# Kernel tuning notes

Hardware: AMD Instinct MI355X
Metric: run time of the kernel (lower is better)

Reference implementation:

```python
import jax, jax.numpy as jnp
import numpy as np
import math

INPUTDIM = 256
OUTDIM = 512
GRIDSIZE = 64

def setup_inputs() -> dict:
    key = jax.random.key(0)
    k1, k2 = jax.random.split(key)
    x = jax.random.normal(k1, (4096, INPUTDIM), dtype=jnp.float32)
    # init: randn / (sqrt(inputdim) * sqrt(gridsize))  (smooth_initialization=False)
    fouriercoeffs = jax.random.normal(k2, (2, OUTDIM, INPUTDIM, GRIDSIZE), dtype=jnp.float32) / (
        math.sqrt(INPUTDIM) * math.sqrt(GRIDSIZE))
    bias = jnp.zeros((1, OUTDIM), dtype=jnp.float32)
    return {"x": x, "fouriercoeffs": fouriercoeffs, "bias": bias}

def reference(x, fouriercoeffs, bias):
    # x: [N, I]; fouriercoeffs: [2, O, I, G]; bias: [1, O]
    k = jnp.arange(1, GRIDSIZE + 1, dtype=x.dtype)          # [G]
    kx = x[:, :, None] * k[None, None, :]                   # [N, I, G]
    c = jnp.cos(kx)
    s = jnp.sin(kx)
    # contraction over (I, G) — GEMM-equivalent of the naive broadcast-sum
    y = jnp.einsum('nig,oig->no', c, fouriercoeffs[0])
    y = y + jnp.einsum('nig,oig->no', s, fouriercoeffs[1])
    y = y + bias
    return y
```

## Files before the change

### kernel.cpp

```cpp
#include <hip/hip_runtime.h>
#include <hip/hip_bf16.h>

#define IDIM 256
#define GDIM 64
#define ODIM 512
#define KD   (IDIM * GDIM)
#define TILE_SHORTS (512 * 64)
#define WS_NEED ((size_t)512 * TILE_SHORTS * 2)

typedef __attribute__((ext_vector_type(8))) short bhalf8;
typedef __attribute__((ext_vector_type(4))) float fvec4;
typedef __attribute__((ext_vector_type(4))) unsigned uvec4;

#define INV2PI 0.15915494309189535f

static __device__ __forceinline__ short bf16b(float v) {
    __hip_bfloat16 hb = __float2bfloat16(v);
    short s; __builtin_memcpy(&s, &hb, 2); return s;
}
static __device__ __forceinline__ unsigned cvtpk(float lo, float hi) {
    unsigned r;
    asm("v_cvt_pk_bf16_f32 %0, %1, %2" : "=v"(r) : "v"(lo), "v"(hi));
    return r;
}

__global__ void prep_b(const float* __restrict__ coeffs, short* __restrict__ ws) {
    const int b = blockIdx.x;
    const int i = b >> 1, h = b & 1;
    const int o = threadIdx.x;
    short* dst = ws + ((size_t)b * 512 + o) * 64;
    const int swz = (o & 7) << 4;
#pragma unroll
    for (int j = 0; j < 8; ++j) {
        const int z = j >> 2, Qq = j & 3;
        const float* src = coeffs + ((size_t)z * ODIM + o) * KD
                         + (size_t)i * GDIM + 16 * Qq + 8 * h;
        fvec4 v0 = ((const fvec4*)src)[0];
        fvec4 v1 = ((const fvec4*)src)[1];
        bhalf8 pk;
#pragma unroll
        for (int u = 0; u < 4; ++u) { pk[u] = bf16b(v0[u]); pk[4 + u] = bf16b(v1[u]); }
        *(bhalf8*)((char*)dst + ((j * 16) ^ swz)) = pk;
    }
}

__global__ void bias_init(const float* __restrict__ bias, float* __restrict__ out) {
    int idx = blockIdx.x * 256 + threadIdx.x;
    fvec4 bv = ((const fvec4*)bias)[idx & 127];
    ((fvec4*)out)[idx] = bv;
}

#define FENCE() do { asm volatile("s_waitcnt vmcnt(0) lgkmcnt(0)" ::: "memory"); \
                     __builtin_amdgcn_sched_barrier(0); \
                     __syncthreads(); } while (0)

#define ADV2(cA,cB,sA,sB,C2) do { \
    float _cn = __builtin_fmaf((C2),(cB),-(cA)); (cA)=(cB); (cB)=_cn; \
    float _sn = __builtin_fmaf((C2),(sB),-(sA)); (sA)=(sB); (sB)=_sn; \
    _cn = __builtin_fmaf((C2),(cB),-(cA)); (cA)=(cB); (cB)=_cn; \
    _sn = __builtin_fmaf((C2),(sB),-(sA)); (sA)=(sB); (sB)=_sn; } while (0)

template<int USE_WS>
__global__ void __launch_bounds__(256, 4)
fkan_gemm(const float* __restrict__ x, const float* __restrict__ coeffs,
          const short* __restrict__ wsb, float* __restrict__ out) {
    __shared__ __align__(16) short B_lds[2][128 * 64];
    __shared__ float  sl_rev[4][128];
    __shared__ float2 sl_cs[4][128];

    const int bx = blockIdx.x;
    const int xcd = bx & 7, j = bx >> 3;
    const int lg  = xcd * 4 + (j & 3);
    const int mt  = j >> 2;
    const int ot  = lg >> 3, ks = lg & 7;
    const int row0 = mt * 128, col0 = ot * 128;
    const int i0 = ks * 32;

    const int t = threadIdx.x;
    const int lane = t & 63, wid = t >> 6;
    const int kl  = (lane >> 4) * 16;
    const int msk = (lane & 7) << 4;
    const int rA0 = wid * 32 + (lane & 15);
    const float m0f = (float)(16 * (lane >> 4) + 1);

    fvec4 acc[2][8];
#pragma unroll
    for (int a = 0; a < 2; ++a)
#pragma unroll
        for (int b = 0; b < 8; ++b) acc[a][b] = (fvec4)0.0f;

    auto fill_sl = [&](int chunk) {
#pragma unroll
        for (int w = 0; w < 2; ++w) {
            int idx = t + w * 256;
            int il2 = idx & 3, r2 = idx >> 2;
            float xv = x[(size_t)(row0 + r2) * IDIM + i0 + chunk * 4 + il2];
            float rev = xv * INV2PI;
            float a = __builtin_amdgcn_fractf(rev);
            float2 cs;
            cs.x = __builtin_amdgcn_cosf(a);
            cs.y = __builtin_amdgcn_sinf(a);
            sl_rev[il2][r2] = rev;
            sl_cs[il2][r2] = cs;
        }
    };

    auto dmaB = [&](int T1) {
        const short* src = wsb + (size_t)(i0 * 2 + T1) * TILE_SHORTS
                         + (size_t)col0 * 64 + (size_t)t * 8;
        const int bsel = T1 & 1;
#pragma unroll
        for (int q = 0; q < 4; ++q)
            __builtin_amdgcn_global_load_lds(
                (const __attribute__((address_space(1))) unsigned*)(src + q * 2048),
                (__attribute__((address_space(3))) unsigned*)
                    &B_lds[bsel][q * 2048 + wid * 512],
                16, 0, 0);
    };

    auto stage_fb = [&](int T1) {
        const int bsel = T1 & 1;
        const int i = i0 + (T1 >> 1), hh = T1 & 1;
        const int o = t >> 1, z = t & 1;
        char* drow = (char*)&B_lds[bsel][o * 64];
        const int swz = (o & 7) << 4;
#pragma unroll
        for (int Qq = 0; Qq < 4; ++Qq) {
            const float* src = coeffs + ((size_t)z * ODIM + col0 + o) * KD
                             + (size_t)i * GDIM + 16 * Qq + 8 * hh;
            fvec4 v0 = ((const fvec4*)src)[0];
            fvec4 v1 = ((const fvec4*)src)[1];
            bhalf8 pk;
#pragma unroll
            for (int u = 0; u < 4; ++u) { pk[u] = bf16b(v0[u]); pk[4 + u] = bf16b(v1[u]); }
            *(bhalf8*)(drow + ((z * 64 + Qq * 16) ^ swz)) = pk;
        }
    };

    fill_sl(0);
    if (USE_WS) dmaB(0);
    FENCE();

    float ccA0, ccB0, csA0, csB0, cC20;
    float ccA1, ccB1, csA1, csB1, cC21;

#pragma unroll 1
    for (int T = 0; T < 64; ++T) {
        if ((T & 7) == 0 && T > 0) {
            fill_sl(T >> 3);
            FENCE();
        }
        if (USE_WS) {
            if (T < 63) dmaB(T + 1);
            __builtin_amdgcn_sched_barrier(0);
        } else {
            stage_fb(T);
            FENCE();
        }

        const int bsel = T & 1;
        const int il = (T >> 1) & 3;
        const short* Bb = &B_lds[bsel][0];

        bhalf8 afc[2], afs[2];
        if ((T & 1) == 0) {
#pragma unroll
            for (int fm = 0; fm < 2; ++fm) {
                const int rr = rA0 + fm * 16;
                float rev = sl_rev[il][rr];
                float2 cs1 = sl_cs[il][rr];
                float C2 = cs1.x + cs1.x;
                float a0 = __builtin_amdgcn_fractf(rev * m0f);
                float cA = __builtin_amdgcn_cosf(a0);
                float sA = __builtin_amdgcn_sinf(a0);
                float cB = __builtin_fmaf(cA, cs1.x, -(sA * cs1.y));
                float sB = __builtin_fmaf(sA, cs1.x,  (cA * cs1.y));
                uvec4 uc, us;
                uc[0] = cvtpk(cA, cB); us[0] = cvtpk(sA, sB);
#pragma unroll
                for (int p = 1; p < 4; ++p) {
                    ADV2(cA, cB, sA, sB, C2);
                    uc[p] = cvtpk(cA, cB); us[p] = cvtpk(sA, sB);
                }
                if (fm == 0) { ccA0 = cA; ccB0 = cB; csA0 = sA; csB0 = sB; cC20 = C2; }
                else         { ccA1 = cA; ccB1 = cB; csA1 = sA; csB1 = sB; cC21 = C2; }
                afc[fm] = __builtin_bit_cast(bhalf8, uc);
                afs[fm] = __builtin_bit_cast(bhalf8, us);
            }
        } else {
#pragma unroll
            for (int fm = 0; fm < 2; ++fm) {
                float cA = fm ? ccA1 : ccA0, cB = fm ? ccB1 : ccB0;
                float sA = fm ? csA1 : csA0, sB = fm ? csB1 : csB0;
                float C2 = fm ? cC21 : cC20;
                uvec4 uc, us;
#pragma unroll
                for (int p = 0; p < 4; ++p) {
                    ADV2(cA, cB, sA, sB, C2);
                    uc[p] = cvtpk(cA, cB); us[p] = cvtpk(sA, sB);
                }
                afc[fm] = __builtin_bit_cast(bhalf8, uc);
                afs[fm] = __builtin_bit_cast(bhalf8, us);
            }
        }

#pragma unroll
        for (int half = 0; half < 2; ++half) {
            bhalf8 bq[4];
#pragma unroll
            for (int f4 = 0; f4 < 4; ++f4)
                bq[f4] = *(const bhalf8*)((const char*)Bb +
                    (size_t)(half * 64 + f4 * 16 + (lane & 15)) * 128 + (kl ^ msk));
            __builtin_amdgcn_s_setprio(1);
#pragma unroll
            for (int fm = 0; fm < 2; ++fm)
#pragma unroll
                for (int f4 = 0; f4 < 4; ++f4)
                    acc[fm][half * 4 + f4] = __builtin_amdgcn_mfma_f32_16x16x32_bf16(
                        afc[fm], bq[f4], acc[fm][half * 4 + f4], 0, 0, 0);
            __builtin_amdgcn_s_setprio(0);
#pragma unroll
            for (int f4 = 0; f4 < 4; ++f4)
                bq[f4] = *(const bhalf8*)((const char*)Bb +
                    (size_t)(half * 64 + f4 * 16 + (lane & 15)) * 128 + ((64 + kl) ^ msk));
            __builtin_amdgcn_s_setprio(1);
#pragma unroll
            for (int fm = 0; fm < 2; ++fm)
#pragma unroll
                for (int f4 = 0; f4 < 4; ++f4)
                    acc[fm][half * 4 + f4] = __builtin_amdgcn_mfma_f32_16x16x32_bf16(
                        afs[fm], bq[f4], acc[fm][half * 4 + f4], 0, 0, 0);
            __builtin_amdgcn_s_setprio(0);
        }

        FENCE();
    }

#pragma unroll
    for (int fm = 0; fm < 2; ++fm) {
#pragma unroll
        for (int f = 0; f < 8; ++f) {
            int col = col0 + f * 16 + (lane & 15);
#pragma unroll
            for (int r = 0; r < 4; ++r) {
                int row = row0 + wid * 32 + fm * 16 + ((lane >> 4) * 4) + r;
                atomicAdd(&out[(size_t)row * ODIM + col], acc[fm][f][r]);
            }
        }
    }
}

extern "C" void kernel_launch(void* const* d_in, const int* in_sizes, int n_in,
                              void* d_out, int out_size, void* d_ws, size_t ws_size,
                              hipStream_t stream) {
    (void)in_sizes; (void)n_in; (void)out_size;
    const float* x      = (const float*)d_in[0];
    const float* coeffs = (const float*)d_in[1];
    const float* bias   = (const float*)d_in[2];
    float* out = (float*)d_out;

    const bool use_ws = (ws_size >= WS_NEED) && (((uintptr_t)d_ws & 15) == 0);

    bias_init<<<dim3(2048), dim3(256), 0, stream>>>(bias, out);
    if (use_ws) {
        prep_b<<<dim3(512), dim3(512), 0, stream>>>(coeffs, (short*)d_ws);
        fkan_gemm<1><<<dim3(1024), dim3(256), 0, stream>>>(x, coeffs, (const short*)d_ws, out);
    } else {
        fkan_gemm<0><<<dim3(1024), dim3(256), 0, stream>>>(x, coeffs, nullptr, out);
    }
}
```

Baseline: 176.7 us.

## Split B tiles into cos/sin halves with 4-deep LDS ring and vmcnt-based pipelining

Restructures the GEMM main loop to stream B in cos and sin half-tiles through a 4-slot LDS ring. Each slot is issued two steps ahead and waited on with partial vmcnt waits plus a bare s_barrier, instead of a full vmcnt/lgkmcnt drain each iteration. The workspace layout and swizzle are changed to 64-byte rows with a 2-bit XOR key, and the cos and sin recurrences are interleaved per half. The aim is to overlap global-to-LDS DMA with MFMA work and cut full-drain barriers. The cost is more barriers per iteration and subtler ordering between the ring slots.

```diff
diff --git a/kernel.cpp b/kernel.cpp
--- a/kernel.cpp
+++ b/kernel.cpp
@@ -5,14 +5,15 @@
 #define GDIM 64
 #define ODIM 512
 #define KD   (IDIM * GDIM)
-#define TILE_SHORTS (512 * 64)
-#define WS_NEED ((size_t)512 * TILE_SHORTS * 2)
+#define WS_NEED ((size_t)512 * 512 * 64 * 2)
 
 typedef __attribute__((ext_vector_type(8))) short bhalf8;
 typedef __attribute__((ext_vector_type(4))) float fvec4;
 typedef __attribute__((ext_vector_type(4))) unsigned uvec4;
 
 #define INV2PI 0.15915494309189535f
+#define AS1 __attribute__((address_space(1)))
+#define AS3 __attribute__((address_space(3)))
 
 static __device__ __forceinline__ short bf16b(float v) {
     __hip_bfloat16 hb = __float2bfloat16(v);
@@ -24,24 +25,37 @@
     return r;
 }
 
+#define ADVP(A,B,C2) do { float _t = __builtin_fmaf((C2),(B),-(A)); (A)=(B); (B)=_t; \
+                          _t = __builtin_fmaf((C2),(B),-(A)); (A)=(B); (B)=_t; } while (0)
+
+#define BOUND(N) do { asm volatile("s_waitcnt vmcnt(" #N ")" ::: "memory"); \
+                      __builtin_amdgcn_sched_barrier(0); \
+                      __builtin_amdgcn_s_barrier(); \
+                      __builtin_amdgcn_sched_barrier(0); } while (0)
+#define BOUND_LG() do { asm volatile("s_waitcnt lgkmcnt(0)" ::: "memory"); \
+                      __builtin_amdgcn_sched_barrier(0); \
+                      __builtin_amdgcn_s_barrier(); \
+                      __builtin_amdgcn_sched_barrier(0); } while (0)
+
 __global__ void prep_b(const float* __restrict__ coeffs, short* __restrict__ ws) {
     const int b = blockIdx.x;
     const int i = b >> 1, h = b & 1;
     const int o = threadIdx.x;
-    short* dst = ws + ((size_t)b * 512 + o) * 64;
-    const int swz = (o & 7) << 4;
-#pragma unroll
-    for (int j = 0; j < 8; ++j) {
-        const int z = j >> 2, Qq = j & 3;
-        const float* src = coeffs + ((size_t)z * ODIM + o) * KD
-                         + (size_t)i * GDIM + 16 * Qq + 8 * h;
-        fvec4 v0 = ((const fvec4*)src)[0];
-        fvec4 v1 = ((const fvec4*)src)[1];
-        bhalf8 pk;
-#pragma unroll
-        for (int u = 0; u < 4; ++u) { pk[u] = bf16b(v0[u]); pk[4 + u] = bf16b(v1[u]); }
-        *(bhalf8*)((char*)dst + ((j * 16) ^ swz)) = pk;
-    }
+    char* dst = (char*)(ws + ((size_t)b * 512 + o) * 64);
+    const int key = (o >> 1) & 3;
+#pragma unroll
+    for (int z = 0; z < 2; ++z)
+#pragma unroll
+        for (int g = 0; g < 4; ++g) {
+            const float* src = coeffs + ((size_t)z * ODIM + o) * KD
+                             + (size_t)i * GDIM + 16 * g + 8 * h;
+            fvec4 v0 = ((const fvec4*)src)[0];
+            fvec4 v1 = ((const fvec4*)src)[1];
+            bhalf8 pk;
+#pragma unroll
+            for (int u = 0; u < 4; ++u) { pk[u] = bf16b(v0[u]); pk[4 + u] = bf16b(v1[u]); }
+            *(bhalf8*)(dst + z * 64 + (((g ^ key)) << 4)) = pk;
+        }
 }
 
 __global__ void bias_init(const float* __restrict__ bias, float* __restrict__ out) {
@@ -50,21 +64,11 @@
     ((fvec4*)out)[idx] = bv;
 }
 
-#define FENCE() do { asm volatile("s_waitcnt vmcnt(0) lgkmcnt(0)" ::: "memory"); \
-                     __builtin_amdgcn_sched_barrier(0); \
-                     __syncthreads(); } while (0)
-
-#define ADV2(cA,cB,sA,sB,C2) do { \
-    float _cn = __builtin_fmaf((C2),(cB),-(cA)); (cA)=(cB); (cB)=_cn; \
-    float _sn = __builtin_fmaf((C2),(sB),-(sA)); (sA)=(sB); (sB)=_sn; \
-    _cn = __builtin_fmaf((C2),(cB),-(cA)); (cA)=(cB); (cB)=_cn; \
-    _sn = __builtin_fmaf((C2),(sB),-(sA)); (sA)=(sB); (sB)=_sn; } while (0)
-
 template<int USE_WS>
 __global__ void __launch_bounds__(256, 4)
 fkan_gemm(const float* __restrict__ x, const float* __restrict__ coeffs,
           const short* __restrict__ wsb, float* __restrict__ out) {
-    __shared__ __align__(16) short B_lds[2][128 * 64];
+    __shared__ __align__(16) short B4[4][4096];
     __shared__ float  sl_rev[4][128];
     __shared__ float2 sl_cs[4][128];
 
@@ -78,10 +82,10 @@
 
     const int t = threadIdx.x;
     const int lane = t & 63, wid = t >> 6;
-    const int kl  = (lane >> 4) * 16;
-    const int msk = (lane & 7) << 4;
+    const int q   = lane >> 4;
+    const int key = ((lane & 15) >> 1) & 3;
     const int rA0 = wid * 32 + (lane & 15);
-    const float m0f = (float)(16 * (lane >> 4) + 1);
+    const float m0f = (float)(16 * q + 1);
 
     fvec4 acc[2][8];
 #pragma unroll
@@ -105,135 +109,168 @@
         }
     };
 
-    auto dmaB = [&](int T1) {
-        const short* src = wsb + (size_t)(i0 * 2 + T1) * TILE_SHORTS
-                         + (size_t)col0 * 64 + (size_t)t * 8;
-        const int bsel = T1 & 1;
-#pragma unroll
-        for (int q = 0; q < 4; ++q)
-            __builtin_amdgcn_global_load_lds(
-                (const __attribute__((address_space(1))) unsigned*)(src + q * 2048),
-                (__attribute__((address_space(3))) unsigned*)
-                    &B_lds[bsel][q * 2048 + wid * 512],
-                16, 0, 0);
+    auto dma_half = [&](int Hh) {
+        const int Tt = Hh >> 1, zz = Hh & 1, bs = Hh & 3;
+        const char* srcl = (const char*)wsb + (((size_t)(i0 * 2 + Tt)) << 16)
+                         + (size_t)(col0 + wid * 32 + (lane >> 2)) * 128
+                         + zz * 64 + (lane & 3) * 16;
+        __builtin_amdgcn_global_load_lds((const AS1 unsigned*)srcl,
+            (AS3 unsigned*)&B4[bs][wid * 1024], 16, 0, 0);
+        __builtin_amdgcn_global_load_lds((const AS1 unsigned*)(srcl + 16 * 128),
+            (AS3 unsigned*)&B4[bs][wid * 1024 + 512], 16, 0, 0);
     };
 
-    auto stage_fb = [&](int T1) {
-        const int bsel = T1 & 1;
-        const int i = i0 + (T1 >> 1), hh = T1 & 1;
-        const int o = t >> 1, z = t & 1;
-        char* drow = (char*)&B_lds[bsel][o * 64];
-        const int swz = (o & 7) << 4;
-#pragma unroll
-        for (int Qq = 0; Qq < 4; ++Qq) {
-            const float* src = coeffs + ((size_t)z * ODIM + col0 + o) * KD
-                             + (size_t)i * GDIM + 16 * Qq + 8 * hh;
+    auto stage_fb = [&](int Tt) {
+        const int hh = Tt & 1, i = i0 + (Tt >> 1);
+        const int o = t >> 1, zz = t & 1;
+        const int keyo = (o >> 1) & 3;
+        char* d0 = (char*)&B4[(2 * Tt + zz) & 3][o * 32];
+#pragma unroll
+        for (int g = 0; g < 4; ++g) {
+            const float* src = coeffs + ((size_t)zz * ODIM + col0 + o) * KD
+                             + (size_t)i * GDIM + 16 * g + 8 * hh;
             fvec4 v0 = ((const fvec4*)src)[0];
             fvec4 v1 = ((const fvec4*)src)[1];
             bhalf8 pk;
 #pragma unroll
             for (int u = 0; u < 4; ++u) { pk[u] = bf16b(v0[u]); pk[4 + u] = bf16b(v1[u]); }
-            *(bhalf8*)(drow + ((z * 64 + Qq * 16) ^ swz)) = pk;
+            *(bhalf8*)(d0 + ((g ^ keyo) << 4)) = pk;
         }
     };
 
+    auto mfma_half = [&](int bs, bhalf8 af0, bhalf8 af1) {
+        const char* Bb = (const char*)&B4[bs][0];
+        const int goff = (q ^ key) << 4;
+#pragma unroll
+        for (int ch = 0; ch < 2; ++ch) {
+            bhalf8 bq[4];
+#pragma unroll
+            for (int j2 = 0; j2 < 4; ++j2)
+                bq[j2] = *(const bhalf8*)(Bb +
+                    (size_t)((lane & 15) + (ch * 4 + j2) * 16) * 64 + goff);
+            __builtin_amdgcn_s_setprio(1);
+#pragma unroll
+            for (int j2 = 0; j2 < 4; ++j2) {
+                acc[0][ch * 4 + j2] = __builtin_amdgcn_mfma_f32_16x16x32_bf16(
+                    af0, bq[j2], acc[0][ch * 4 + j2], 0, 0, 0);
+                acc[1][ch * 4 + j2] = __builtin_amdgcn_mfma_f32_16x16x32_bf16(
+                    af1, bq[j2], acc[1][ch * 4 + j2], 0, 0, 0);
+            }
+            __builtin_amdgcn_s_setprio(0);
+        }
+    };
+
+    float ccA0, ccB0, ccA1, ccB1;
+    float ssA0, ssB0, ssA1, ssB1;
+    float C20, C21;
+
     fill_sl(0);
-    if (USE_WS) dmaB(0);
-    FENCE();
-
-    float ccA0, ccB0, csA0, csB0, cC20;
-    float ccA1, ccB1, csA1, csB1, cC21;
+    if (USE_WS) {
+        dma_half(0); dma_half(1);
+        BOUND(2);
+    } else {
+        stage_fb(0);
+        __syncthreads();
+    }
 
 #pragma unroll 1
-    for (int T = 0; T < 64; ++T) {
-        if ((T & 7) == 0 && T > 0) {
-            fill_sl(T >> 3);
-            FENCE();
-        }
+    for (int H4 = 0; H4 < 32; ++H4) {
+        const int Hb = H4 * 4;
+        const int il = H4 & 3;
+        bhalf8 af[2];
+
         if (USE_WS) {
-            if (T < 63) dmaB(T + 1);
-            __builtin_amdgcn_sched_barrier(0);
+            if (Hb > 0) {
+                if ((Hb & 15) == 0) {
+                    BOUND(2);
+                    fill_sl(Hb >> 4);
+                    BOUND_LG();
+                } else {
+                    BOUND(2);
+                }
+            }
+            dma_half(Hb + 2);
         } else {
-            stage_fb(T);
-            FENCE();
-        }
-
-        const int bsel = T & 1;
-        const int il = (T >> 1) & 3;
-        const short* Bb = &B_lds[bsel][0];
-
-        bhalf8 afc[2], afs[2];
-        if ((T & 1) == 0) {
-#pragma unroll
-            for (int fm = 0; fm < 2; ++fm) {
-                const int rr = rA0 + fm * 16;
-                float rev = sl_rev[il][rr];
-                float2 cs1 = sl_cs[il][rr];
-                float C2 = cs1.x + cs1.x;
-                float a0 = __builtin_amdgcn_fractf(rev * m0f);
-                float cA = __builtin_amdgcn_cosf(a0);
-                float sA = __builtin_amdgcn_sinf(a0);
-                float cB = __builtin_fmaf(cA, cs1.x, -(sA * cs1.y));
-                float sB = __builtin_fmaf(sA, cs1.x,  (cA * cs1.y));
-                uvec4 uc, us;
-                uc[0] = cvtpk(cA, cB); us[0] = cvtpk(sA, sB);
-#pragma unroll
-                for (int p = 1; p < 4; ++p) {
-                    ADV2(cA, cB, sA, sB, C2);
-                    uc[p] = cvtpk(cA, cB); us[p] = cvtpk(sA, sB);
-                }
-                if (fm == 0) { ccA0 = cA; ccB0 = cB; csA0 = sA; csB0 = sB; cC20 = C2; }
-                else         { ccA1 = cA; ccB1 = cB; csA1 = sA; csB1 = sB; cC21 = C2; }
-                afc[fm] = __builtin_bit_cast(bhalf8, uc);
-                afs[fm] = __builtin_bit_cast(bhalf8, us);
+            if (Hb > 0) {
+                __syncthreads();
+                if ((Hb & 15) == 0) fill_sl(Hb >> 4);
+                stage_fb(Hb >> 1);
+                __syncthreads();
             }
+        }
+#pragma unroll
+        for (int fm = 0; fm < 2; ++fm) {
+            const int rr = rA0 + fm * 16;
+            float rev = sl_rev[il][rr];
+            float2 cs1 = sl_cs[il][rr];
+            float C2x = cs1.x + cs1.x;
+            float a0 = __builtin_amdgcn_fractf(rev * m0f);
+            float c0 = __builtin_amdgcn_cosf(a0);
+            float s0 = __builtin_amdgcn_sinf(a0);
+            float cBv = __builtin_fmaf(c0, cs1.x, -(s0 * cs1.y));
+            float sBv = __builtin_fmaf(s0, cs1.x,  c0 * cs1.y);
+            uvec4 u; u[0] = cvtpk(c0, cBv);
+            float A = c0, B = cBv;
+            ADVP(A, B, C2x); u[1] = cvtpk(A, B);
+            ADVP(A, B, C2x); u[2] = cvtpk(A, B);
+            ADVP(A, B, C2x); u[3] = cvtpk(A, B);
+            if (fm == 0) { ccA0 = A; ccB0 = B; ssA0 = s0; ssB0 = sBv; C20 = C2x; }
+            else         { ccA1 = A; ccB1 = B; ssA1 = s0; ssB1 = sBv; C21 = C2x; }
+            af[fm] = __builtin_bit_cast(bhalf8, u);
+        }
+        mfma_half(Hb & 3, af[0], af[1]);
+
+        if (USE_WS) { BOUND(2); dma_half(Hb + 3); }
+#pragma unroll
+        for (int fm = 0; fm < 2; ++fm) {
+            float A = fm ? ssA1 : ssA0, B = fm ? ssB1 : ssB0;
+            float C2x = fm ? C21 : C20;
+            uvec4 u; u[0] = cvtpk(A, B);
+            ADVP(A, B, C2x); u[1] = cvtpk(A, B);
+            ADVP(A, B, C2x); u[2] = cvtpk(A, B);
+            ADVP(A, B, C2x); u[3] = cvtpk(A, B);
+            if (fm == 0) { ssA0 = A; ssB0 = B; } else { ssA1 = A; ssB1 = B; }
+            af[fm] = __builtin_bit_cast(bhalf8, u);
+        }
+        mfma_half((Hb + 1) & 3, af[0], af[1]);
+
+        if (USE_WS) {
+            BOUND(2);
+            if (Hb + 4 < 128) dma_half(Hb + 4);
         } else {
-#pragma unroll
-            for (int fm = 0; fm < 2; ++fm) {
-                float cA = fm ? ccA1 : ccA0, cB = fm ? ccB1 : ccB0;
-                float sA = fm ? csA1 : csA0, sB = fm ? csB1 : csB0;
-                float C2 = fm ? cC21 : cC20;
-                uvec4 uc, us;
-#pragma unroll
-                for (int p = 0; p < 4; ++p) {
-                    ADV2(cA, cB, sA, sB, C2);
-                    uc[p] = cvtpk(cA, cB); us[p] = cvtpk(sA, sB);
-                }
-                afc[fm] = __builtin_bit_cast(bhalf8, uc);
-                afs[fm] = __builtin_bit_cast(bhalf8, us);
-            }
-        }
-
-#pragma unroll
-        for (int half = 0; half < 2; ++half) {
-            bhalf8 bq[4];
-#pragma unroll
-            for (int f4 = 0; f4 < 4; ++f4)
-                bq[f4] = *(const bhalf8*)((const char*)Bb +
-                    (size_t)(half * 64 + f4 * 16 + (lane & 15)) * 128 + (kl ^ msk));
-            __builtin_amdgcn_s_setprio(1);
-#pragma unroll
-            for (int fm = 0; fm < 2; ++fm)
-#pragma unroll
-                for (int f4 = 0; f4 < 4; ++f4)
-                    acc[fm][half * 4 + f4] = __builtin_amdgcn_mfma_f32_16x16x32_bf16(
-                        afc[fm], bq[f4], acc[fm][half * 4 + f4], 0, 0, 0);
-            __builtin_amdgcn_s_setprio(0);
-#pragma unroll
-            for (int f4 = 0; f4 < 4; ++f4)
-                bq[f4] = *(const bhalf8*)((const char*)Bb +
-                    (size_t)(half * 64 + f4 * 16 + (lane & 15)) * 128 + ((64 + kl) ^ msk));
-            __builtin_amdgcn_s_setprio(1);
-#pragma unroll
-            for (int fm = 0; fm < 2; ++fm)
-#pragma unroll
-                for (int f4 = 0; f4 < 4; ++f4)
-                    acc[fm][half * 4 + f4] = __builtin_amdgcn_mfma_f32_16x16x32_bf16(
-                        afs[fm], bq[f4], acc[fm][half * 4 + f4], 0, 0, 0);
-            __builtin_amdgcn_s_setprio(0);
-        }
-
-        FENCE();
+            __syncthreads();
+            stage_fb((Hb >> 1) + 1);
+            __syncthreads();
+        }
+#pragma unroll
+        for (int fm = 0; fm < 2; ++fm) {
+            float A = fm ? ccA1 : ccA0, B = fm ? ccB1 : ccB0;
+            float C2x = fm ? C21 : C20;
+            uvec4 u;
+            ADVP(A, B, C2x); u[0] = cvtpk(A, B);
+            ADVP(A, B, C2x); u[1] = cvtpk(A, B);
+            ADVP(A, B, C2x); u[2] = cvtpk(A, B);
+            ADVP(A, B, C2x); u[3] = cvtpk(A, B);
+            af[fm] = __builtin_bit_cast(bhalf8, u);
+        }
+        mfma_half((Hb + 2) & 3, af[0], af[1]);
+
+        if (USE_WS) {
+            BOUND(2);
+            if (Hb + 5 < 128) dma_half(Hb + 5);
+        }
+#pragma unroll
+        for (int fm = 0; fm < 2; ++fm) {
+            float A = fm ? ssA1 : ssA0, B = fm ? ssB1 : ssB0;
+            float C2x = fm ? C21 : C20;
+            uvec4 u;
+            ADVP(A, B, C2x); u[0] = cvtpk(A, B);
+            ADVP(A, B, C2x); u[1] = cvtpk(A, B);
+            ADVP(A, B, C2x); u[2] = cvtpk(A, B);
+            ADVP(A, B, C2x); u[3] = cvtpk(A, B);
+            af[fm] = __builtin_bit_cast(bhalf8, u);
+        }
+        mfma_half((Hb + 3) & 3, af[0], af[1]);
     }
 
 #pragma unroll
```

Result: slower. 190.1 us (+7.6%).

## Software-pipeline cos/sin generation with MFMA and make sine table per-wave

Applied to the files above, without the earlier changes.

Restructures the main loop so the cosine A-fragments for the next step are generated after the current step's MFMAs, and the sine fragments are computed between the cosine and sine MFMA batches. This interleaves VALU recurrence work with matrix work. The per-chunk fill of the sine/cosine seed table now covers only each wave's own rows and is issued two steps ahead, which removes its extra block barrier. Register pressure rises because the fragments and recurrence state stay live across iterations, and the recurrence order changes slightly.

```diff
diff --git a/kernel.cpp b/kernel.cpp
--- a/kernel.cpp
+++ b/kernel.cpp
@@ -13,6 +13,8 @@
 typedef __attribute__((ext_vector_type(4))) unsigned uvec4;
 
 #define INV2PI 0.15915494309189535f
+#define AS1 __attribute__((address_space(1)))
+#define AS3 __attribute__((address_space(3)))
 
 static __device__ __forceinline__ short bf16b(float v) {
     __hip_bfloat16 hb = __float2bfloat16(v);
@@ -23,6 +25,9 @@
     asm("v_cvt_pk_bf16_f32 %0, %1, %2" : "=v"(r) : "v"(lo), "v"(hi));
     return r;
 }
+
+#define ADVP(A,B,C2) do { float _t = __builtin_fmaf((C2),(B),-(A)); (A)=(B); (B)=_t; \
+                          _t = __builtin_fmaf((C2),(B),-(A)); (A)=(B); (B)=_t; } while (0)
 
 __global__ void prep_b(const float* __restrict__ coeffs, short* __restrict__ ws) {
     const int b = blockIdx.x;
@@ -54,12 +59,6 @@
                      __builtin_amdgcn_sched_barrier(0); \
                      __syncthreads(); } while (0)
 
-#define ADV2(cA,cB,sA,sB,C2) do { \
-    float _cn = __builtin_fmaf((C2),(cB),-(cA)); (cA)=(cB); (cB)=_cn; \
-    float _sn = __builtin_fmaf((C2),(sB),-(sA)); (sA)=(sB); (sB)=_sn; \
-    _cn = __builtin_fmaf((C2),(cB),-(cA)); (cA)=(cB); (cB)=_cn; \
-    _sn = __builtin_fmaf((C2),(sB),-(sA)); (sA)=(sB); (sB)=_sn; } while (0)
-
 template<int USE_WS>
 __global__ void __launch_bounds__(256, 4)
 fkan_gemm(const float* __restrict__ x, const float* __restrict__ coeffs,
@@ -91,9 +90,9 @@
 
     auto fill_sl = [&](int chunk) {
 #pragma unroll
-        for (int w = 0; w < 2; ++w) {
-            int idx = t + w * 256;
-            int il2 = idx & 3, r2 = idx >> 2;
+        for (int w2 = 0; w2 < 2; ++w2) {
+            int idx = lane + w2 * 64;
+            int il2 = idx & 3, r2 = wid * 32 + (idx >> 2);
             float xv = x[(size_t)(row0 + r2) * IDIM + i0 + chunk * 4 + il2];
             float rev = xv * INV2PI;
             float a = __builtin_amdgcn_fractf(rev);
@@ -112,9 +111,8 @@
 #pragma unroll
         for (int q = 0; q < 4; ++q)
             __builtin_amdgcn_global_load_lds(
-                (const __attribute__((address_space(1))) unsigned*)(src + q * 2048),
-                (__attribute__((address_space(3))) unsigned*)
-                    &B_lds[bsel][q * 2048 + wid * 512],
+                (const AS1 unsigned*)(src + q * 2048),
+                (AS3 unsigned*)&B_lds[bsel][q * 2048 + wid * 512],
                 16, 0, 0);
     };
 
@@ -137,103 +135,124 @@
         }
     };
 
+    float ccA0, ccB0, ccA1, ccB1;
+    float ssA0, ssB0, ssA1, ssB1;
+    float C20, C21;
+    bhalf8 afc[2], afs[2];
+
+    auto seed_even = [&](int Te) {
+        const int il = (Te >> 1) & 3;
+#pragma unroll
+        for (int fm = 0; fm < 2; ++fm) {
+            const int rr = rA0 + fm * 16;
+            float rev = sl_rev[il][rr];
+            float2 cs1 = sl_cs[il][rr];
+            float C2x = cs1.x + cs1.x;
+            float a0 = __builtin_amdgcn_fractf(rev * m0f);
+            float c0 = __builtin_amdgcn_cosf(a0);
+            float s0 = __builtin_amdgcn_sinf(a0);
+            float cBv = __builtin_fmaf(c0, cs1.x, -(s0 * cs1.y));
+            float sBv = __builtin_fmaf(s0, cs1.x,  c0 * cs1.y);
+            uvec4 u; u[0] = cvtpk(c0, cBv);
+            float A = c0, B = cBv;
+            ADVP(A, B, C2x); u[1] = cvtpk(A, B);
+            ADVP(A, B, C2x); u[2] = cvtpk(A, B);
+            ADVP(A, B, C2x); u[3] = cvtpk(A, B);
+            if (fm == 0) { ccA0 = A; ccB0 = B; ssA0 = s0; ssB0 = sBv; C20 = C2x; }
+            else         { ccA1 = A; ccB1 = B; ssA1 = s0; ssB1 = sBv; C21 = C2x; }
+            afc[fm] = __builtin_bit_cast(bhalf8, u);
+        }
+    };
+
+    auto mfma_z = [&](const char* Bb, int z, bhalf8 a0f, bhalf8 a1f) {
+        const int koff = (z * 64 + kl) ^ msk;
+#pragma unroll
+        for (int half = 0; half < 2; ++half) {
+            bhalf8 bq[4];
+#pragma unroll
+            for (int f4 = 0; f4 < 4; ++f4)
+                bq[f4] = *(const bhalf8*)(Bb +
+                    (size_t)(half * 64 + f4 * 16 + (lane & 15)) * 128 + koff);
+            __builtin_amdgcn_s_setprio(1);
+#pragma unroll
+            for (int f4 = 0; f4 < 4; ++f4) {
+                acc[0][half * 4 + f4] = __builtin_amdgcn_mfma_f32_16x16x32_bf16(
+                    a0f, bq[f4], acc[0][half * 4 + f4], 0, 0, 0);
+                acc[1][half * 4 + f4] = __builtin_amdgcn_mfma_f32_16x16x32_bf16(
+                    a1f, bq[f4], acc[1][half * 4 + f4], 0, 0, 0);
+            }
+            __builtin_amdgcn_s_setprio(0);
+        }
+    };
+
     fill_sl(0);
-    if (USE_WS) dmaB(0);
-    FENCE();
-
-    float ccA0, ccB0, csA0, csB0, cC20;
-    float ccA1, ccB1, csA1, csB1, cC21;
+    asm volatile("s_waitcnt lgkmcnt(0)" ::: "memory");
+    __builtin_amdgcn_sched_barrier(0);
+    seed_even(0);
+    if (USE_WS) { dmaB(0); FENCE(); }
+    else        { __syncthreads(); }
 
 #pragma unroll 1
     for (int T = 0; T < 64; ++T) {
-        if ((T & 7) == 0 && T > 0) {
-            fill_sl(T >> 3);
-            FENCE();
-        }
         if (USE_WS) {
+            if ((T & 7) == 6 && T < 62) fill_sl((T + 2) >> 3);
             if (T < 63) dmaB(T + 1);
             __builtin_amdgcn_sched_barrier(0);
         } else {
+            if ((T & 7) == 6 && T < 62) fill_sl((T + 2) >> 3);
             stage_fb(T);
-            FENCE();
-        }
-
-        const int bsel = T & 1;
-        const int il = (T >> 1) & 3;
-        const short* Bb = &B_lds[bsel][0];
-
-        bhalf8 afc[2], afs[2];
+            __syncthreads();
+        }
+
+        const char* Bb = (const char*)&B_lds[T & 1][0];
+
+        mfma_z(Bb, 0, afc[0], afc[1]);
         if ((T & 1) == 0) {
 #pragma unroll
             for (int fm = 0; fm < 2; ++fm) {
-                const int rr = rA0 + fm * 16;
-                float rev = sl_rev[il][rr];
-                float2 cs1 = sl_cs[il][rr];
-                float C2 = cs1.x + cs1.x;
-                float a0 = __builtin_amdgcn_fractf(rev * m0f);
-                float cA = __builtin_amdgcn_cosf(a0);
-                float sA = __builtin_amdgcn_sinf(a0);
-                float cB = __builtin_fmaf(cA, cs1.x, -(sA * cs1.y));
-                float sB = __builtin_fmaf(sA, cs1.x,  (cA * cs1.y));
-                uvec4 uc, us;
-                uc[0] = cvtpk(cA, cB); us[0] = cvtpk(sA, sB);
-#pragma unroll
-                for (int p = 1; p < 4; ++p) {
-                    ADV2(cA, cB, sA, sB, C2);
-                    uc[p] = cvtpk(cA, cB); us[p] = cvtpk(sA, sB);
+                float A = fm ? ssA1 : ssA0, B = fm ? ssB1 : ssB0;
+                float C2x = fm ? C21 : C20;
+                uvec4 u; u[0] = cvtpk(A, B);
+                ADVP(A, B, C2x); u[1] = cvtpk(A, B);
+                ADVP(A, B, C2x); u[2] = cvtpk(A, B);
+                ADVP(A, B, C2x); u[3] = cvtpk(A, B);
+                if (fm == 0) { ssA0 = A; ssB0 = B; } else { ssA1 = A; ssB1 = B; }
+                afs[fm] = __builtin_bit_cast(bhalf8, u);
+            }
+        } else {
+#pragma unroll
+            for (int fm = 0; fm < 2; ++fm) {
+                float A = fm ? ssA1 : ssA0, B = fm ? ssB1 : ssB0;
+                float C2x = fm ? C21 : C20;
+                uvec4 u;
+                ADVP(A, B, C2x); u[0] = cvtpk(A, B);
+                ADVP(A, B, C2x); u[1] = cvtpk(A, B);
+                ADVP(A, B, C2x); u[2] = cvtpk(A, B);
+                ADVP(A, B, C2x); u[3] = cvtpk(A, B);
+                afs[fm] = __builtin_bit_cast(bhalf8, u);
+            }
+        }
+
+        mfma_z(Bb, 1, afs[0], afs[1]);
+        if (T < 63) {
+            if ((T & 1) == 0) {
+#pragma unroll
+                for (int fm = 0; fm < 2; ++fm) {
+                    float A = fm ? ccA1 : ccA0, B = fm ? ccB1 : ccB0;
+                    float C2x = fm ? C21 : C20;
+                    uvec4 u;
+                    ADVP(A, B, C2x); u[0] = cvtpk(A, B);
+                    ADVP(A, B, C2x); u[1] = cvtpk(A, B);
+                    ADVP(A, B, C2x); u[2] = cvtpk(A, B);
+                    ADVP(A, B, C2x); u[3] = cvtpk(A, B);
+                    afc[fm] = __builtin_bit_cast(bhalf8, u);
                 }
-                if (fm == 0) { ccA0 = cA; ccB0 = cB; csA0 = sA; csB0 = sB; cC20 = C2; }
-                else         { ccA1 = cA; ccB1 = cB; csA1 = sA; csB1 = sB; cC21 = C2; }
-                afc[fm] = __builtin_bit_cast(bhalf8, uc);
-                afs[fm] = __builtin_bit_cast(bhalf8, us);
-            }
-        } else {
-#pragma unroll
-            for (int fm = 0; fm < 2; ++fm) {
-                float cA = fm ? ccA1 : ccA0, cB = fm ? ccB1 : ccB0;
-                float sA = fm ? csA1 : csA0, sB = fm ? csB1 : csB0;
-                float C2 = fm ? cC21 : cC20;
-                uvec4 uc, us;
-#pragma unroll
-                for (int p = 0; p < 4; ++p) {
-                    ADV2(cA, cB, sA, sB, C2);
-                    uc[p] = cvtpk(cA, cB); us[p] = cvtpk(sA, sB);
-                }
-                afc[fm] = __builtin_bit_cast(bhalf8, uc);
-                afs[fm] = __builtin_bit_cast(bhalf8, us);
-            }
-        }
-
-#pragma unroll
-        for (int half = 0; half < 2; ++half) {
-            bhalf8 bq[4];
-#pragma unroll
-            for (int f4 = 0; f4 < 4; ++f4)
-                bq[f4] = *(const bhalf8*)((const char*)Bb +
-                    (size_t)(half * 64 + f4 * 16 + (lane & 15)) * 128 + (kl ^ msk));
-            __builtin_amdgcn_s_setprio(1);
-#pragma unroll
-            for (int fm = 0; fm < 2; ++fm)
-#pragma unroll
-                for (int f4 = 0; f4 < 4; ++f4)
-                    acc[fm][half * 4 + f4] = __builtin_amdgcn_mfma_f32_16x16x32_bf16(
-                        afc[fm], bq[f4], acc[fm][half * 4 + f4], 0, 0, 0);
-            __builtin_amdgcn_s_setprio(0);
-#pragma unroll
-            for (int f4 = 0; f4 < 4; ++f4)
-                bq[f4] = *(const bhalf8*)((const char*)Bb +
-                    (size_t)(half * 64 + f4 * 16 + (lane & 15)) * 128 + ((64 + kl) ^ msk));
-            __builtin_amdgcn_s_setprio(1);
-#pragma unroll
-            for (int fm = 0; fm < 2; ++fm)
-#pragma unroll
-                for (int f4 = 0; f4 < 4; ++f4)
-                    acc[fm][half * 4 + f4] = __builtin_amdgcn_mfma_f32_16x16x32_bf16(
-                        afs[fm], bq[f4], acc[fm][half * 4 + f4], 0, 0, 0);
-            __builtin_amdgcn_s_setprio(0);
-        }
-
-        FENCE();
+            } else {
+                seed_even(T + 1);
+            }
+        }
+
+        if (USE_WS) FENCE(); else __syncthreads();
     }
 
 #pragma unroll
```

New measurement: 176.1 us. Within noise of the previous version (-0.3%).
